# Kernel tuning notes

Measured on AMD Instinct MI355X. Metric: run time of the kernel, lower is better.

Reference implementation:

```python
import jax, jax.numpy as jnp
import numpy as np


def _binarize_act(z):
    # STE: forward = sign(z), backward = d/dz clamp(z,-1,1)
    clipped = jnp.clip(z, -1.0, 1.0)
    return jax.lax.stop_gradient(jnp.sign(z) - clipped) + clipped


def _binarize_weight(w):
    # per-output-channel scaling factor = mean |w| over (in, kh, kw), detached
    scale = jax.lax.stop_gradient(jnp.mean(jnp.abs(w), axis=(1, 2, 3), keepdims=True))
    clipped = jnp.clip(w, -1.0, 1.0)
    return jax.lax.stop_gradient(scale * jnp.sign(w) - clipped) + clipped


def setup_inputs() -> dict:
    key = jax.random.key(0)
    k = jax.random.split(key, 6)
    B, C, H, W = 16, 64, 256, 256
    return {
        "x": jax.random.normal(k[0], (B, C, H, W), dtype=jnp.float32),
        "move0_bias": jax.random.normal(k[1], (1, C, 1, 1), dtype=jnp.float32) * 0.1,
        "conv_weight": jax.random.normal(k[2], (C, C, 3, 3), dtype=jnp.float32) * 0.1,
        "prelu_weight": jnp.full((C,), 0.25, dtype=jnp.float32)
        + jax.random.normal(k[3], (C,), dtype=jnp.float32) * 0.01,
        "pr_bias0": jax.random.normal(k[4], (1, C, 1, 1), dtype=jnp.float32) * 0.1,
        "pr_bias1": jax.random.normal(k[5], (1, C, 1, 1), dtype=jnp.float32) * 0.1,
    }


def reference(x, move0_bias, conv_weight, prelu_weight, pr_bias0, pr_bias1):
    identity = x  # stride=1, out_channels == in_channels -> no downsample / concat
    z = _binarize_act(x + move0_bias)
    bw = _binarize_weight(conv_weight)
    y = jax.lax.conv_general_dilated(
        z, bw, window_strides=(1, 1), padding=((1, 1), (1, 1)),
        dimension_numbers=("NCHW", "OIHW", "NCHW"))
    # RPReLU: bias0 -> per-channel PReLU -> bias1
    y = y + pr_bias0
    a = prelu_weight.reshape(1, -1, 1, 1)
    y = jnp.where(y > 0, y, a * y)
    y = y + pr_bias1
    return y + identity
```

## Files before the change

kernel.cpp:

```cpp
#include <hip/hip_runtime.h>
#include <stdint.h>

#define Bn 16
#define C 64
#define H 256
#define W 256
#define HW (H * W)
#define NHW (Bn * HW)

#define TW 64
#define TH 16
#define SZH 18
#define SZW 73

typedef float f32x4 __attribute__((ext_vector_type(4)));

__global__ void prep_weights(const float* __restrict__ w,
                             uint64_t* __restrict__ wbits,
                             float* __restrict__ scale,
                             int* __restrict__ edgeL,
                             int* __restrict__ edgeR) {
    int o = blockIdx.x;
    int c = threadIdx.x;
    const float* wp = w + ((size_t)o * C + c) * 9;
    float asum = 0.f;
    uint64_t m[9];
#pragma unroll
    for (int tap = 0; tap < 9; ++tap) {
        float v = wp[tap];
        asum += fabsf(v);
        m[tap] = __ballot(v > 0.f);
    }
    if (c == 0) {
#pragma unroll
        for (int tap = 0; tap < 9; ++tap) wbits[o * 9 + tap] = m[tap];
        edgeL[o] = 2 * (int)(__popcll(m[0]) + __popcll(m[3]) + __popcll(m[6]));
        edgeR[o] = 2 * (int)(__popcll(m[2]) + __popcll(m[5]) + __popcll(m[8]));
    }
#pragma unroll
    for (int off = 32; off > 0; off >>= 1)
        asum += __shfl_down(asum, off);
    if (c == 0) scale[o] = asum * (1.f / 576.f);
}

__global__ __launch_bounds__(256) void bconv_fused(
        const uint64_t* __restrict__ wbits,
        const float* __restrict__ scale,
        const int* __restrict__ edgeL,
        const int* __restrict__ edgeR,
        const float* __restrict__ x,
        const float* __restrict__ bias,
        const float* __restrict__ pb0,
        const float* __restrict__ aw,
        const float* __restrict__ pb1,
        float* __restrict__ out) {
    __shared__ uint64_t swb[640];
    __shared__ uint64_t sz[SZH * SZW];
    __shared__ float4 sprm[C];
    __shared__ float sbias[C];
    __shared__ int sEL[C], sER[C];

    int t = threadIdx.x;
    if (t < C) {
        sprm[t] = make_float4(scale[t], pb0[t], aw[t], pb1[t]);
        sbias[t] = bias[t];
        sEL[t] = edgeL[t];
        sER[t] = edgeR[t];
    }
    for (int i = t; i < 576; i += 256) {
        int o = i / 9;
        swb[o * 10 + (i - o * 9)] = wbits[i];
    }

    int bid = blockIdx.x;
    int n = bid >> 6;
    int tile = bid & 63;
    int ty = tile >> 2, tx = tile & 3;
    int gh0 = ty * TH, gw0 = tx * TW;

    const float* xn = x + (size_t)n * C * HW;

    __syncthreads();

    for (int ci = t; ci < SZH * 18; ci += 256) {
        int r = ci / 18;
        int cb = (ci - r * 18) * 4;
        int gh = gh0 + r - 1;
        int gwb = gw0 - 4 + cb;
        uint64_t b0 = 0, b1 = 0, b2 = 0, b3 = 0;
        if ((unsigned)gh < (unsigned)H && (unsigned)gwb < (unsigned)(W - 3)) {
            const float* xp = xn + gh * W + gwb;
#pragma unroll 8
            for (int ch = 0; ch < C; ++ch) {
                f32x4 v = *reinterpret_cast<const f32x4*>(xp + (size_t)ch * HW);
                float bc = sbias[ch];
                b0 |= (uint64_t)(v.x + bc > 0.f) << ch;
                b1 |= (uint64_t)(v.y + bc > 0.f) << ch;
                b2 |= (uint64_t)(v.z + bc > 0.f) << ch;
                b3 |= (uint64_t)(v.w + bc > 0.f) << ch;
            }
        }
        uint64_t* zp = &sz[r * SZW + cb];
        zp[0] = b0; zp[1] = b1; zp[2] = b2; zp[3] = b3;
    }
    __syncthreads();

    int tr = t >> 4;
    int tc4 = (t & 15) * 4;
    int gh = gh0 + tr;
    int gw = gw0 + tc4;

    uint64_t zb[3][6];
#pragma unroll
    for (int i = 0; i < 3; ++i)
#pragma unroll
        for (int j = 0; j < 6; ++j)
            zb[i][j] = sz[(tr + i) * SZW + tc4 + 3 + j];

    const float* xid = xn + gh * W + gw;
    float* op = out + (size_t)n * C * HW + gh * W + gw;
    bool leftE  = (gw == 0);
    bool rightE = (gw == W - 4);

    if (gh >= 1 && gh <= H - 2) {
        f32x4 id0 = *reinterpret_cast<const f32x4*>(xid);
        f32x4 id1 = *reinterpret_cast<const f32x4*>(xid + HW);
#pragma unroll 2
        for (int o = 0; o < C; ++o) {
            const uint64_t* wp = &swb[o * 10];
            int s0 = 0, s1 = 0, s2 = 0, s3 = 0;
#pragma unroll
            for (int i = 0; i < 3; ++i)
#pragma unroll
                for (int jj = 0; jj < 3; ++jj) {
                    uint64_t wt = wp[i * 3 + jj];
                    s0 += (int)__popcll(wt ^ zb[i][jj]);
                    s1 += (int)__popcll(wt ^ zb[i][jj + 1]);
                    s2 += (int)__popcll(wt ^ zb[i][jj + 2]);
                    s3 += (int)__popcll(wt ^ zb[i][jj + 3]);
                }
            int d0 = 576 - 2 * s0, d1 = 576 - 2 * s1;
            int d2 = 576 - 2 * s2, d3 = 576 - 2 * s3;
            if (leftE)  d0 += sEL[o] - 192;
            if (rightE) d3 += sER[o] - 192;

            float4 pr = sprm[o];
            f32x4 idv = id0;
            id0 = id1;
            if (o < C - 2)
                id1 = *reinterpret_cast<const f32x4*>(xid + (size_t)(o + 2) * HW);
            f32x4 r;
            float y;
            y = pr.x * (float)d0 + pr.y; y = y > 0.f ? y : pr.z * y; r.x = y + pr.w + idv.x;
            y = pr.x * (float)d1 + pr.y; y = y > 0.f ? y : pr.z * y; r.y = y + pr.w + idv.y;
            y = pr.x * (float)d2 + pr.y; y = y > 0.f ? y : pr.z * y; r.z = y + pr.w + idv.z;
            y = pr.x * (float)d3 + pr.y; y = y > 0.f ? y : pr.z * y; r.w = y + pr.w + idv.w;
            __builtin_nontemporal_store(r, reinterpret_cast<f32x4*>(op + (size_t)o * HW));
        }
    } else {
        int vrow[3], vcol[6];
#pragma unroll
        for (int i = 0; i < 3; ++i)
            vrow[i] = ((unsigned)(gh - 1 + i) < (unsigned)H) ? -1 : 0;
#pragma unroll
        for (int j = 0; j < 6; ++j)
            vcol[j] = ((unsigned)(gw - 1 + j) < (unsigned)W) ? -1 : 0;
        int nv[4];
#pragma unroll
        for (int q = 0; q < 4; ++q) {
            int nr = (vrow[0] & 1) + (vrow[1] & 1) + (vrow[2] & 1);
            int nc = (vcol[q] & 1) + (vcol[q + 1] & 1) + (vcol[q + 2] & 1);
            nv[q] = nr * nc;
        }
#pragma unroll 2
        for (int o = 0; o < C; ++o) {
            const uint64_t* wp = &swb[o * 10];
            int s[4] = {0, 0, 0, 0};
#pragma unroll
            for (int i = 0; i < 3; ++i)
#pragma unroll
                for (int jj = 0; jj < 3; ++jj) {
                    uint64_t wt = wp[i * 3 + jj];
#pragma unroll
                    for (int q = 0; q < 4; ++q)
                        s[q] += (vrow[i] & vcol[q + jj]) &
                                (int)__popcll(wt ^ zb[i][q + jj]);
                }
            float4 pr = sprm[o];
            f32x4 idv = *reinterpret_cast<const f32x4*>(xid + (size_t)o * HW);
            f32x4 r;
            float y;
            y = pr.x * (float)(64 * nv[0] - 2 * s[0]) + pr.y; y = y > 0.f ? y : pr.z * y; r.x = y + pr.w + idv.x;
            y = pr.x * (float)(64 * nv[1] - 2 * s[1]) + pr.y; y = y > 0.f ? y : pr.z * y; r.y = y + pr.w + idv.y;
            y = pr.x * (float)(64 * nv[2] - 2 * s[2]) + pr.y; y = y > 0.f ? y : pr.z * y; r.z = y + pr.w + idv.z;
            y = pr.x * (float)(64 * nv[3] - 2 * s[3]) + pr.y; y = y > 0.f ? y : pr.z * y; r.w = y + pr.w + idv.w;
            __builtin_nontemporal_store(r, reinterpret_cast<f32x4*>(op + (size_t)o * HW));
        }
    }
}

extern "C" void kernel_launch(void* const* d_in, const int* in_sizes, int n_in,
                              void* d_out, int out_size, void* d_ws, size_t ws_size,
                              hipStream_t stream) {
    const float* x           = (const float*)d_in[0];
    const float* move0_bias  = (const float*)d_in[1];
    const float* conv_weight = (const float*)d_in[2];
    const float* prelu_w     = (const float*)d_in[3];
    const float* pr_bias0    = (const float*)d_in[4];
    const float* pr_bias1    = (const float*)d_in[5];
    float* out = (float*)d_out;

    uint8_t* ws = (uint8_t*)d_ws;
    uint64_t* wbits = (uint64_t*)ws;
    float* scale    = (float*)(ws + 4608);
    int* edgeL      = (int*)(ws + 4864);
    int* edgeR      = (int*)(ws + 5120);

    prep_weights<<<64, 64, 0, stream>>>(conv_weight, wbits, scale, edgeL, edgeR);
    bconv_fused<<<Bn * (H / TH) * (W / TW), 256, 0, stream>>>(
        wbits, scale, edgeL, edgeR, x, move0_bias,
        pr_bias0, prelu_w, pr_bias1, out);
}
```

Baseline: 567.8 us.

## Double threads per tile, two pixels per thread, read params from global

```diff
diff --git a/kernel.cpp b/kernel.cpp
--- a/kernel.cpp
+++ b/kernel.cpp
@@ -14,6 +14,7 @@
 #define SZW 73
 
 typedef float f32x4 __attribute__((ext_vector_type(4)));
+typedef float f32x2 __attribute__((ext_vector_type(2)));
 
 __global__ void prep_weights(const float* __restrict__ w,
                              uint64_t* __restrict__ wbits,
@@ -43,7 +44,7 @@
     if (c == 0) scale[o] = asum * (1.f / 576.f);
 }
 
-__global__ __launch_bounds__(256) void bconv_fused(
+__global__ __launch_bounds__(512, 8) void bconv_fused(
         const uint64_t* __restrict__ wbits,
         const float* __restrict__ scale,
         const int* __restrict__ edgeL,
@@ -54,24 +55,9 @@
         const float* __restrict__ aw,
         const float* __restrict__ pb1,
         float* __restrict__ out) {
-    __shared__ uint64_t swb[640];
     __shared__ uint64_t sz[SZH * SZW];
-    __shared__ float4 sprm[C];
-    __shared__ float sbias[C];
-    __shared__ int sEL[C], sER[C];
 
     int t = threadIdx.x;
-    if (t < C) {
-        sprm[t] = make_float4(scale[t], pb0[t], aw[t], pb1[t]);
-        sbias[t] = bias[t];
-        sEL[t] = edgeL[t];
-        sER[t] = edgeR[t];
-    }
-    for (int i = t; i < 576; i += 256) {
-        int o = i / 9;
-        swb[o * 10 + (i - o * 9)] = wbits[i];
-    }
-
     int bid = blockIdx.x;
     int n = bid >> 6;
     int tile = bid & 63;
@@ -80,20 +66,18 @@
 
     const float* xn = x + (size_t)n * C * HW;
 
-    __syncthreads();
-
-    for (int ci = t; ci < SZH * 18; ci += 256) {
-        int r = ci / 18;
-        int cb = (ci - r * 18) * 4;
+    if (t < SZH * 18) {
+        int r = t / 18;
+        int cb = (t - r * 18) * 4;
         int gh = gh0 + r - 1;
         int gwb = gw0 - 4 + cb;
         uint64_t b0 = 0, b1 = 0, b2 = 0, b3 = 0;
-        if ((unsigned)gh < (unsigned)H && (unsigned)gwb < (unsigned)(W - 3)) {
+        if ((unsigned)gh < (unsigned)H && (unsigned)gwb <= (unsigned)(W - 4)) {
             const float* xp = xn + gh * W + gwb;
 #pragma unroll 8
             for (int ch = 0; ch < C; ++ch) {
                 f32x4 v = *reinterpret_cast<const f32x4*>(xp + (size_t)ch * HW);
-                float bc = sbias[ch];
+                float bc = bias[ch];
                 b0 |= (uint64_t)(v.x + bc > 0.f) << ch;
                 b1 |= (uint64_t)(v.y + bc > 0.f) << ch;
                 b2 |= (uint64_t)(v.z + bc > 0.f) << ch;
@@ -105,30 +89,32 @@
     }
     __syncthreads();
 
-    int tr = t >> 4;
-    int tc4 = (t & 15) * 4;
+    int tr = t >> 5;
+    int tc2 = (t & 31) * 2;
     int gh = gh0 + tr;
-    int gw = gw0 + tc4;
+    int gw = gw0 + tc2;
 
-    uint64_t zb[3][6];
+    uint64_t zb[3][4];
 #pragma unroll
     for (int i = 0; i < 3; ++i)
 #pragma unroll
-        for (int j = 0; j < 6; ++j)
-            zb[i][j] = sz[(tr + i) * SZW + tc4 + 3 + j];
+        for (int j = 0; j < 4; ++j)
+            zb[i][j] = sz[(tr + i) * SZW + tc2 + 3 + j];
 
     const float* xid = xn + gh * W + gw;
     float* op = out + (size_t)n * C * HW + gh * W + gw;
     bool leftE  = (gw == 0);
-    bool rightE = (gw == W - 4);
+    bool rightE = (gw == W - 2);
 
-    if (gh >= 1 && gh <= H - 2) {
-        f32x4 id0 = *reinterpret_cast<const f32x4*>(xid);
-        f32x4 id1 = *reinterpret_cast<const f32x4*>(xid + HW);
+    bool slowW = (ty == 0 && tr < 2) || (ty == 15 && tr >= 14);
+
+    if (!slowW) {
+        f32x2 id0 = *reinterpret_cast<const f32x2*>(xid);
+        f32x2 id1 = *reinterpret_cast<const f32x2*>(xid + HW);
 #pragma unroll 2
         for (int o = 0; o < C; ++o) {
-            const uint64_t* wp = &swb[o * 10];
-            int s0 = 0, s1 = 0, s2 = 0, s3 = 0;
+            const uint64_t* wp = wbits + o * 9;
+            int s0 = 0, s1 = 0;
 #pragma unroll
             for (int i = 0; i < 3; ++i)
 #pragma unroll
@@ -136,65 +122,52 @@
                     uint64_t wt = wp[i * 3 + jj];
                     s0 += (int)__popcll(wt ^ zb[i][jj]);
                     s1 += (int)__popcll(wt ^ zb[i][jj + 1]);
-                    s2 += (int)__popcll(wt ^ zb[i][jj + 2]);
-                    s3 += (int)__popcll(wt ^ zb[i][jj + 3]);
                 }
             int d0 = 576 - 2 * s0, d1 = 576 - 2 * s1;
-            int d2 = 576 - 2 * s2, d3 = 576 - 2 * s3;
-            if (leftE)  d0 += sEL[o] - 192;
-            if (rightE) d3 += sER[o] - 192;
+            if (leftE)  d0 += edgeL[o] - 192;
+            if (rightE) d1 += edgeR[o] - 192;
 
-            float4 pr = sprm[o];
-            f32x4 idv = id0;
+            float sc = scale[o], bb0 = pb0[o], af = aw[o], bb1 = pb1[o];
+            f32x2 idv = id0;
             id0 = id1;
             if (o < C - 2)
-                id1 = *reinterpret_cast<const f32x4*>(xid + (size_t)(o + 2) * HW);
-            f32x4 r;
+                id1 = *reinterpret_cast<const f32x2*>(xid + (size_t)(o + 2) * HW);
+            f32x2 r;
             float y;
-            y = pr.x * (float)d0 + pr.y; y = y > 0.f ? y : pr.z * y; r.x = y + pr.w + idv.x;
-            y = pr.x * (float)d1 + pr.y; y = y > 0.f ? y : pr.z * y; r.y = y + pr.w + idv.y;
-            y = pr.x * (float)d2 + pr.y; y = y > 0.f ? y : pr.z * y; r.z = y + pr.w + idv.z;
-            y = pr.x * (float)d3 + pr.y; y = y > 0.f ? y : pr.z * y; r.w = y + pr.w + idv.w;
-            __builtin_nontemporal_store(r, reinterpret_cast<f32x4*>(op + (size_t)o * HW));
+            y = sc * (float)d0 + bb0; y = y > 0.f ? y : af * y; r.x = y + bb1 + idv.x;
+            y = sc * (float)d1 + bb0; y = y > 0.f ? y : af * y; r.y = y + bb1 + idv.y;
+            __builtin_nontemporal_store(r, reinterpret_cast<f32x2*>(op + (size_t)o * HW));
         }
     } else {
-        int vrow[3], vcol[6];
+        int vrow[3], vcol[4];
 #pragma unroll
         for (int i = 0; i < 3; ++i)
             vrow[i] = ((unsigned)(gh - 1 + i) < (unsigned)H) ? -1 : 0;
 #pragma unroll
-        for (int j = 0; j < 6; ++j)
+        for (int j = 0; j < 4; ++j)
             vcol[j] = ((unsigned)(gw - 1 + j) < (unsigned)W) ? -1 : 0;
-        int nv[4];
-#pragma unroll
-        for (int q = 0; q < 4; ++q) {
-            int nr = (vrow[0] & 1) + (vrow[1] & 1) + (vrow[2] & 1);
-            int nc = (vcol[q] & 1) + (vcol[q + 1] & 1) + (vcol[q + 2] & 1);
-            nv[q] = nr * nc;
-        }
+        int nr  = (vrow[0] & 1) + (vrow[1] & 1) + (vrow[2] & 1);
+        int nv0 = nr * ((vcol[0] & 1) + (vcol[1] & 1) + (vcol[2] & 1));
+        int nv1 = nr * ((vcol[1] & 1) + (vcol[2] & 1) + (vcol[3] & 1));
 #pragma unroll 2
         for (int o = 0; o < C; ++o) {
-            const uint64_t* wp = &swb[o * 10];
-            int s[4] = {0, 0, 0, 0};
+            const uint64_t* wp = wbits + o * 9;
+            int s0 = 0, s1 = 0;
 #pragma unroll
             for (int i = 0; i < 3; ++i)
 #pragma unroll
                 for (int jj = 0; jj < 3; ++jj) {
                     uint64_t wt = wp[i * 3 + jj];
-#pragma unroll
-                    for (int q = 0; q < 4; ++q)
-                        s[q] += (vrow[i] & vcol[q + jj]) &
-                                (int)__popcll(wt ^ zb[i][q + jj]);
+                    s0 += (vrow[i] & vcol[jj])     & (int)__popcll(wt ^ zb[i][jj]);
+                    s1 += (vrow[i] & vcol[jj + 1]) & (int)__popcll(wt ^ zb[i][jj + 1]);
                 }
-            float4 pr = sprm[o];
-            f32x4 idv = *reinterpret_cast<const f32x4*>(xid + (size_t)o * HW);
-            f32x4 r;
+            float sc = scale[o], bb0 = pb0[o], af = aw[o], bb1 = pb1[o];
+            f32x2 idv = *reinterpret_cast<const f32x2*>(xid + (size_t)o * HW);
+            f32x2 r;
             float y;
-            y = pr.x * (float)(64 * nv[0] - 2 * s[0]) + pr.y; y = y > 0.f ? y : pr.z * y; r.x = y + pr.w + idv.x;
-            y = pr.x * (float)(64 * nv[1] - 2 * s[1]) + pr.y; y = y > 0.f ? y : pr.z * y; r.y = y + pr.w + idv.y;
-            y = pr.x * (float)(64 * nv[2] - 2 * s[2]) + pr.y; y = y > 0.f ? y : pr.z * y; r.z = y + pr.w + idv.z;
-            y = pr.x * (float)(64 * nv[3] - 2 * s[3]) + pr.y; y = y > 0.f ? y : pr.z * y; r.w = y + pr.w + idv.w;
-            __builtin_nontemporal_store(r, reinterpret_cast<f32x4*>(op + (size_t)o * HW));
+            y = sc * (float)(64 * nv0 - 2 * s0) + bb0; y = y > 0.f ? y : af * y; r.x = y + bb1 + idv.x;
+            y = sc * (float)(64 * nv1 - 2 * s1) + bb0; y = y > 0.f ? y : af * y; r.y = y + bb1 + idv.y;
+            __builtin_nontemporal_store(r, reinterpret_cast<f32x2*>(op + (size_t)o * HW));
         }
     }
 }
@@ -217,7 +190,7 @@
     int* edgeR      = (int*)(ws + 5120);
 
     prep_weights<<<64, 64, 0, stream>>>(conv_weight, wbits, scale, edgeL, edgeR);
-    bconv_fused<<<Bn * (H / TH) * (W / TW), 256, 0, stream>>>(
+    bconv_fused<<<Bn * (H / TH) * (W / TW), 512, 0, stream>>>(
         wbits, scale, edgeL, edgeR, x, move0_bias,
         pr_bias0, prelu_w, pr_bias1, out);
 }
```

Result: no change. 559.9 us (-1.4%).
